# Performance work log

Hardware: AMD Instinct MI355X
Metric: run time of the kernel (lower is better)

## Reference

```python
import jax, jax.numpy as jnp
import numpy as np

B, T, H = 32, 2048, 1024

def setup_inputs() -> dict:
    key = jax.random.key(0)
    ks = jax.random.split(key, 8)
    s = 1.0 / np.sqrt(H)
    return {
        "query": jax.random.normal(ks[0], (B, H), dtype=jnp.float32),
        "values": jax.random.normal(ks[1], (B, T, H), dtype=jnp.float32),
        "Wq": jax.random.uniform(ks[2], (H, H), jnp.float32, -s, s),
        "bq": jax.random.uniform(ks[3], (H,), jnp.float32, -s, s),
        "Wv": jax.random.uniform(ks[4], (H, H), jnp.float32, -s, s),
        "bv": jax.random.uniform(ks[5], (H,), jnp.float32, -s, s),
        "Vw": jax.random.uniform(ks[6], (1, H), jnp.float32, -s, s),
        "Vb": jax.random.uniform(ks[7], (1,), jnp.float32, -s, s),
    }

def reference(query, values, Wq, bq, Wv, bv, Vw, Vb):
    # q_proj: [B,1,H], v_proj: [B,T,H]
    q_proj = (query @ Wq.T + bq)[:, None, :]
    v_proj = jnp.einsum('bth,oh->bto', values, Wv) + bv
    # score: [B,T,1] = tanh(...) @ Vw.T + Vb
    score = jnp.einsum('bth,oh->bto', jnp.tanh(q_proj + v_proj), Vw) + Vb
    attention_weights = jax.nn.softmax(score, axis=1)  # over time
    context_vector = jnp.sum(attention_weights * values, axis=1)  # [B,H]
    return (context_vector, attention_weights)
```

## Files before the change

### kernel.cpp

```cpp
#include <hip/hip_runtime.h>

#define BATCH 32
#define TT    2048
#define HH    1024
#define MTOT  (BATCH * TT)

typedef unsigned short ushort_t;
typedef short sh8 __attribute__((ext_vector_type(8)));
typedef float f4 __attribute__((ext_vector_type(4)));
typedef unsigned short us8 __attribute__((ext_vector_type(8)));

__device__ __forceinline__ ushort_t f2bf(float f) {
    unsigned u = __float_as_uint(f);
    u = (u + 0x7fffu + ((u >> 16) & 1u)) >> 16;
    return (ushort_t)u;
}
__device__ __forceinline__ float bf2f(ushort_t h) {
    return __uint_as_float(((unsigned)h) << 16);
}
__device__ __forceinline__ float fast_tanh(float x) {
    float e = __expf(2.0f * x);
    return 1.0f - 2.0f * __builtin_amdgcn_rcpf(e + 1.0f);
}

__device__ __forceinline__ void glds16(const void* g, void* l) {
    __builtin_amdgcn_global_load_lds(
        (const __attribute__((address_space(1))) void*)g,
        (__attribute__((address_space(3))) void*)l, 16, 0, 0);
}

__global__ void cvt_bf16_k(const float* __restrict__ in, ushort_t* __restrict__ out, long n) {
    long i = ((long)blockIdx.x * blockDim.x + threadIdx.x) * 8;
    if (i + 8 > n) return;
    float4 a = *(const float4*)(in + i);
    float4 b = *(const float4*)(in + i + 4);
    us8 o;
    o[0]=f2bf(a.x); o[1]=f2bf(a.y); o[2]=f2bf(a.z); o[3]=f2bf(a.w);
    o[4]=f2bf(b.x); o[5]=f2bf(b.y); o[6]=f2bf(b.z); o[7]=f2bf(b.w);
    *(us8*)(out + i) = o;
}

__global__ void qproj_k(const float* __restrict__ query, const float* __restrict__ Wq,
                        const float* __restrict__ bq, const float* __restrict__ bv,
                        float* __restrict__ qp) {
    int o = blockIdx.x, tid = threadIdx.x;
    float4 w4 = *(const float4*)(Wq + (long)o * HH + tid * 4);
    __shared__ float sm[BATCH][4];
    int wid = tid >> 6, lane = tid & 63;
    for (int b = 0; b < BATCH; ++b) {
        float4 q4 = *(const float4*)(query + (long)b * HH + tid * 4);
        float p = q4.x*w4.x + q4.y*w4.y + q4.z*w4.z + q4.w*w4.w;
        #pragma unroll
        for (int m = 1; m < 64; m <<= 1) p += __shfl_xor(p, m);
        if (lane == 0) sm[b][wid] = p;
    }
    __syncthreads();
    if (tid < BATCH) {
        float s = sm[tid][0] + sm[tid][1] + sm[tid][2] + sm[tid][3] + bq[o] + bv[o];
        qp[(long)tid * HH + o] = s;
    }
}

#define BM 128
#define BN 128
#define BK 64

__global__ __launch_bounds__(256, 2) void score_gemm_k(
    const ushort_t* __restrict__ A, const ushort_t* __restrict__ Bw,
    const float* __restrict__ qp, const float* __restrict__ Vw,
    float* __restrict__ score)
{
    __shared__ ushort_t As[BM * BK];
    __shared__ ushort_t Bs[BN * BK];
    int tid = threadIdx.x;

    int bx = blockIdx.x;
    int x  = bx & 7;
    int s  = bx >> 3;
    int nt = s & 7;
    int mt = ((s >> 3) << 3) | x;
    const long m0 = (long)mt * BM;
    const int  n0 = nt * BN;

    int wid  = tid >> 6, lane = tid & 63;
    int quad = lane >> 4, l16 = lane & 15;
    int wrow = (wid >> 1) * 64, wcol = (wid & 1) * 64;

    f4 acc[4][4] = {};

    int srow = tid >> 3;
    int sseg = tid & 7;
    int xseg = sseg ^ (srow & 7);
    const ushort_t* Ag = A  + (m0 + srow) * (long)HH + xseg * 8;
    const ushort_t* Bg = Bw + (long)(n0 + srow) * HH + xseg * 8;
    char* AsB = (char*)As;
    char* BsB = (char*)Bs;
    const int ldsOff = wid * 1024;

    for (int kt = 0; kt < HH / BK; ++kt) {
        const int kb = kt * BK;
        #pragma unroll
        for (int c = 0; c < 4; ++c) {
            glds16(Ag + (long)c * 32 * HH + kb, AsB + c * 4096 + ldsOff);
            glds16(Bg + (long)c * 32 * HH + kb, BsB + c * 4096 + ldsOff);
        }
        __syncthreads();

        sh8 af[4][2], bf[4][2];
        #pragma unroll
        for (int i = 0; i < 4; ++i) {
            int r = wrow + i * 16 + l16;
            #pragma unroll
            for (int kq = 0; kq < 2; ++kq) {
                int sg = (kq * 4 + quad) ^ (r & 7);
                af[i][kq] = *(const sh8*)(AsB + r * 128 + sg * 16);
            }
        }
        #pragma unroll
        for (int j = 0; j < 4; ++j) {
            int r = wcol + j * 16 + l16;
            #pragma unroll
            for (int kq = 0; kq < 2; ++kq) {
                int sg = (kq * 4 + quad) ^ (r & 7);
                bf[j][kq] = *(const sh8*)(BsB + r * 128 + sg * 16);
            }
        }
        #pragma unroll
        for (int kq = 0; kq < 2; ++kq)
            #pragma unroll
            for (int i = 0; i < 4; ++i)
                #pragma unroll
                for (int j = 0; j < 4; ++j)
                    acc[i][j] = __builtin_amdgcn_mfma_f32_16x16x32_bf16(
                        af[i][kq], bf[j][kq], acc[i][j], 0, 0, 0);
        __syncthreads();
    }

    int bidx = (int)(m0 >> 11);
    const float* qpb = qp + (long)bidx * HH;
    float qv[4], vw[4];
    #pragma unroll
    for (int j = 0; j < 4; ++j) {
        int cg = n0 + wcol + j * 16 + l16;
        qv[j] = qpb[cg];
        vw[j] = Vw[cg];
    }
    #pragma unroll
    for (int i = 0; i < 4; ++i) {
        #pragma unroll
        for (int r = 0; r < 4; ++r) {
            float sum = 0.0f;
            #pragma unroll
            for (int j = 0; j < 4; ++j) {
                float xv = acc[i][j][r] + qv[j];
                sum += fast_tanh(xv) * vw[j];
            }
            sum += __shfl_xor(sum, 1);
            sum += __shfl_xor(sum, 2);
            sum += __shfl_xor(sum, 4);
            sum += __shfl_xor(sum, 8);
            if (l16 == 0) {
                atomicAdd(score + m0 + wrow + i * 16 + quad * 4 + r, sum);
            }
        }
    }
}

__global__ void softmax_k(const float* __restrict__ sc, float* __restrict__ w) {
    int b = blockIdx.x, tid = threadIdx.x;
    const float* s = sc + (long)b * TT;
    float v[8];
    float4 a0 = *(const float4*)(s + tid * 8);
    float4 a1 = *(const float4*)(s + tid * 8 + 4);
    v[0]=a0.x; v[1]=a0.y; v[2]=a0.z; v[3]=a0.w;
    v[4]=a1.x; v[5]=a1.y; v[6]=a1.z; v[7]=a1.w;
    float mx = v[0];
    #pragma unroll
    for (int i = 1; i < 8; ++i) mx = fmaxf(mx, v[i]);
    #pragma unroll
    for (int m = 1; m < 64; m <<= 1) mx = fmaxf(mx, __shfl_xor(mx, m));
    __shared__ float smx[4], ssum[4];
    int wid = tid >> 6;
    if ((tid & 63) == 0) smx[wid] = mx;
    __syncthreads();
    mx = fmaxf(fmaxf(smx[0], smx[1]), fmaxf(smx[2], smx[3]));
    float sum = 0.0f;
    #pragma unroll
    for (int i = 0; i < 8; ++i) { v[i] = __expf(v[i] - mx); sum += v[i]; }
    #pragma unroll
    for (int m = 1; m < 64; m <<= 1) sum += __shfl_xor(sum, m);
    if ((tid & 63) == 0) ssum[wid] = sum;
    __syncthreads();
    sum = ssum[0] + ssum[1] + ssum[2] + ssum[3];
    float inv = 1.0f / sum;
    float4 o0 = make_float4(v[0]*inv, v[1]*inv, v[2]*inv, v[3]*inv);
    float4 o1 = make_float4(v[4]*inv, v[5]*inv, v[6]*inv, v[7]*inv);
    *(float4*)(w + (long)b * TT + tid * 8)     = o0;
    *(float4*)(w + (long)b * TT + tid * 8 + 4) = o1;
}

__global__ void context_k2(const ushort_t* __restrict__ vb, const float* __restrict__ w,
                           float* __restrict__ partial) {
    int b = blockIdx.x, tc = blockIdx.y;
    int tid = threadIdx.x;
    int toff = tid >> 7;
    int hi   = tid & 127;
    int h    = hi * 8;
    __shared__ float sw[128];
    __shared__ float red[128][8];
    if (tid < 128) sw[tid] = w[(long)b * TT + tc * 128 + tid];
    __syncthreads();

    const ushort_t* base = vb + ((long)b * TT + tc * 128 + toff) * HH + h;
    float acc[8] = {0.f,0.f,0.f,0.f,0.f,0.f,0.f,0.f};
    #pragma unroll 8
    for (int it = 0; it < 64; ++it) {
        us8 v = *(const us8*)(base + (long)it * 2 * HH);
        float wt = sw[it * 2 + toff];
        #pragma unroll
        for (int e = 0; e < 8; ++e) acc[e] += wt * bf2f(v[e]);
    }
    if (toff == 1) {
        #pragma unroll
        for (int e = 0; e < 8; ++e) red[hi][e] = acc[e];
    }
    __syncthreads();
    if (toff == 0) {
        #pragma unroll
        for (int e = 0; e < 8; ++e) acc[e] += red[hi][e];
        float* p = partial + ((long)tc * 32 + b) * HH + h;
        *(float4*)(p)     = make_float4(acc[0], acc[1], acc[2], acc[3]);
        *(float4*)(p + 4) = make_float4(acc[4], acc[5], acc[6], acc[7]);
    }
}

__global__ void context_red_k(const float* __restrict__ partial, float* __restrict__ ctx) {
    int i = blockIdx.x * 256 + threadIdx.x;
    float s = 0.f;
    #pragma unroll
    for (int tc = 0; tc < 16; ++tc) s += partial[(long)tc * 32768 + i];
    ctx[i] = s;
}

extern "C" void kernel_launch(void* const* d_in, const int* in_sizes, int n_in,
                              void* d_out, int out_size, void* d_ws, size_t ws_size,
                              hipStream_t stream) {
    const float* query  = (const float*)d_in[0];
    const float* values = (const float*)d_in[1];
    const float* Wq     = (const float*)d_in[2];
    const float* bq     = (const float*)d_in[3];
    const float* Wv     = (const float*)d_in[4];
    const float* bv     = (const float*)d_in[5];
    const float* Vw     = (const float*)d_in[6];

    char* ws = (char*)d_ws;
    ushort_t* vb   = (ushort_t*)ws;
    ushort_t* wvb  = (ushort_t*)(ws + 134217728);
    float*    qp   = (float*)   (ws + 134217728 + 2097152);
    float*    scre = (float*)   (ws + 134217728 + 2097152 + 131072);
    float*    partial = (float*)wvb;

    float* ctx  = (float*)d_out;
    float* wout = (float*)d_out + BATCH * HH;

    hipMemsetAsync(scre, 0, (size_t)MTOT * 4, stream);

    cvt_bf16_k<<<(BATCH * TT * HH) / 2048, 256, 0, stream>>>(values, vb, (long)BATCH * TT * HH);
    cvt_bf16_k<<<(HH * HH) / 2048, 256, 0, stream>>>(Wv, wvb, (long)HH * HH);

    qproj_k<<<HH, 256, 0, stream>>>(query, Wq, bq, bv, qp);

    score_gemm_k<<<(MTOT / BM) * (HH / BN), 256, 0, stream>>>(vb, wvb, qp, Vw, scre);

    softmax_k<<<BATCH, 256, 0, stream>>>(scre, wout);

    context_k2<<<dim3(BATCH, 16), 256, 0, stream>>>(vb, wout, partial);
    context_red_k<<<(BATCH * HH) / 256, 256, 0, stream>>>(partial, ctx);
}
```

Measured before the change: 569.8 us.

## Rewrite score GEMM as 256x256 double-buffered pipelined kernel with 8 waves

Replaces the 128x128 single-buffered bf16 MFMA GEMM with a 256x256 tile using 512 threads, double-buffered LDS, and a hand-scheduled ping-pong pipeline. Global-to-LDS loads for the next K slice are interleaved with MFMA quadrants, coordinated by explicit barriers, waitcnt and setprio. The goal is to hide load latency and raise data reuse per block. It uses 128KB of LDS per block, which limits occupancy and makes the code fragile about waitcnt correctness.

```diff
diff --git a/kernel.cpp b/kernel.cpp
--- a/kernel.cpp
+++ b/kernel.cpp
@@ -61,79 +61,126 @@
     }
 }
 
-#define BM 128
-#define BN 128
-#define BK 64
-
-__global__ __launch_bounds__(256, 2) void score_gemm_k(
+
+#define PBAR()  __builtin_amdgcn_s_barrier()
+#define LGKM0() asm volatile("s_waitcnt lgkmcnt(0)" ::: "memory")
+#define VMW(n)  asm volatile("s_waitcnt vmcnt(" #n ")" ::: "memory")
+#define PRIO(p) __builtin_amdgcn_s_setprio(p)
+
+__device__ __forceinline__ void stage_half(const ushort_t* __restrict__ gbase,
+                                           long row0, int kb,
+                                           char* ldsbase, int h, int w8, int lane) {
+    #pragma unroll
+    for (int c = 0; c < 2; ++c) {
+        int r  = h * 128 + c * 64 + w8 + (lane >> 3);
+        int sg = (lane & 7) ^ (r & 7);
+        glds16(gbase + (row0 + r) * (long)HH + kb + sg * 8,
+               ldsbase + (h * 128 + c * 64 + w8) * 128);
+    }
+}
+
+#define READ_A(Lp, ibase)                                                        \
+    { _Pragma("unroll") for (int i2_ = 0; i2_ < 4; ++i2_) {                      \
+        int r_ = wr * 128 + ((ibase) + i2_) * 16 + l16;                          \
+        _Pragma("unroll") for (int kq_ = 0; kq_ < 2; ++kq_)                      \
+            af[i2_][kq_] = *(const sh8*)((Lp) + r_ * 128 +                       \
+                                          ((((kq_ * 4) + quad) ^ (r_ & 7)) * 16)); } }
+
+#define READ_B(Lp, jbase)                                                        \
+    { _Pragma("unroll") for (int j2_ = 0; j2_ < 2; ++j2_) {                      \
+        int r_ = wc * 64 + ((jbase) + j2_) * 16 + l16;                           \
+        _Pragma("unroll") for (int kq_ = 0; kq_ < 2; ++kq_)                      \
+            bf[(jbase) + j2_][kq_] = *(const sh8*)((Lp) + r_ * 128 +             \
+                                          ((((kq_ * 4) + quad) ^ (r_ & 7)) * 16)); } }
+
+#define MFMA_Q(ibase, jbase)                                                     \
+    { _Pragma("unroll") for (int kq_ = 0; kq_ < 2; ++kq_) {                      \
+      _Pragma("unroll") for (int i2_ = 0; i2_ < 4; ++i2_) {                      \
+      _Pragma("unroll") for (int j2_ = 0; j2_ < 2; ++j2_) {                      \
+            acc[(ibase) + i2_][(jbase) + j2_] =                                  \
+                __builtin_amdgcn_mfma_f32_16x16x32_bf16(                         \
+                    af[i2_][kq_], bf[(jbase) + j2_][kq_],                        \
+                    acc[(ibase) + i2_][(jbase) + j2_], 0, 0, 0); } } } }
+
+__global__ __launch_bounds__(512, 2) void score_gemm_k(
     const ushort_t* __restrict__ A, const ushort_t* __restrict__ Bw,
     const float* __restrict__ qp, const float* __restrict__ Vw,
     float* __restrict__ score)
 {
-    __shared__ ushort_t As[BM * BK];
-    __shared__ ushort_t Bs[BN * BK];
-    int tid = threadIdx.x;
-
-    int bx = blockIdx.x;
-    int x  = bx & 7;
-    int s  = bx >> 3;
-    int nt = s & 7;
-    int mt = ((s >> 3) << 3) | x;
-    const long m0 = (long)mt * BM;
-    const int  n0 = nt * BN;
-
-    int wid  = tid >> 6, lane = tid & 63;
-    int quad = lane >> 4, l16 = lane & 15;
-    int wrow = (wid >> 1) * 64, wcol = (wid & 1) * 64;
-
-    f4 acc[4][4] = {};
-
-    int srow = tid >> 3;
-    int sseg = tid & 7;
-    int xseg = sseg ^ (srow & 7);
-    const ushort_t* Ag = A  + (m0 + srow) * (long)HH + xseg * 8;
-    const ushort_t* Bg = Bw + (long)(n0 + srow) * HH + xseg * 8;
-    char* AsB = (char*)As;
-    char* BsB = (char*)Bs;
-    const int ldsOff = wid * 1024;
-
-    for (int kt = 0; kt < HH / BK; ++kt) {
-        const int kb = kt * BK;
-        #pragma unroll
-        for (int c = 0; c < 4; ++c) {
-            glds16(Ag + (long)c * 32 * HH + kb, AsB + c * 4096 + ldsOff);
-            glds16(Bg + (long)c * 32 * HH + kb, BsB + c * 4096 + ldsOff);
-        }
-        __syncthreads();
-
-        sh8 af[4][2], bf[4][2];
-        #pragma unroll
-        for (int i = 0; i < 4; ++i) {
-            int r = wrow + i * 16 + l16;
-            #pragma unroll
-            for (int kq = 0; kq < 2; ++kq) {
-                int sg = (kq * 4 + quad) ^ (r & 7);
-                af[i][kq] = *(const sh8*)(AsB + r * 128 + sg * 16);
-            }
-        }
-        #pragma unroll
-        for (int j = 0; j < 4; ++j) {
-            int r = wcol + j * 16 + l16;
-            #pragma unroll
-            for (int kq = 0; kq < 2; ++kq) {
-                int sg = (kq * 4 + quad) ^ (r & 7);
-                bf[j][kq] = *(const sh8*)(BsB + r * 128 + sg * 16);
-            }
-        }
-        #pragma unroll
-        for (int kq = 0; kq < 2; ++kq)
-            #pragma unroll
-            for (int i = 0; i < 4; ++i)
-                #pragma unroll
-                for (int j = 0; j < 4; ++j)
-                    acc[i][j] = __builtin_amdgcn_mfma_f32_16x16x32_bf16(
-                        af[i][kq], bf[j][kq], acc[i][j], 0, 0, 0);
-        __syncthreads();
+    __shared__ ushort_t As[2][256 * 64];
+    __shared__ ushort_t Bs[2][256 * 64];
+    const int tid  = threadIdx.x;
+    const int w    = tid >> 6, lane = tid & 63;
+    const int quad = lane >> 4, l16 = lane & 15;
+    const int wr   = w >> 2, wc = w & 3;
+    const int w8   = w << 3;
+
+    int bx   = blockIdx.x;
+    int wgid = (bx & 7) * 128 + (bx >> 3);
+    int mt   = wgid >> 2, nt = wgid & 3;
+    const long m0 = (long)mt * 256;
+    const long n0 = (long)nt * 256;
+
+    char* As0 = (char*)&As[0][0];
+    char* As1 = (char*)&As[1][0];
+    char* Bs0 = (char*)&Bs[0][0];
+    char* Bs1 = (char*)&Bs[1][0];
+
+    f4  acc[8][4] = {};
+    sh8 af[4][2], bf[4][2];
+
+    stage_half(A,  m0, 0,  As0, 0, w8, lane);
+    stage_half(A,  m0, 0,  As0, 1, w8, lane);
+    stage_half(Bw, n0, 0,  Bs0, 0, w8, lane);
+    stage_half(Bw, n0, 0,  Bs0, 1, w8, lane);
+    stage_half(Bw, n0, 64, Bs1, 0, w8, lane);
+    stage_half(Bw, n0, 64, Bs1, 1, w8, lane);
+    VMW(4); PBAR();
+
+    for (int it = 0; it < 7; ++it) {
+        const int kb1 = (2 * it + 1) * 64;
+        const int kb2 = (2 * it + 2) * 64;
+        const int kb3 = (2 * it + 3) * 64;
+        READ_A(As0, 0); READ_B(Bs0, 0);
+        stage_half(A, m0, kb1, As1, 0, w8, lane);
+        PBAR(); LGKM0(); PRIO(1); MFMA_Q(0, 0); PRIO(0); PBAR();
+        READ_B(Bs0, 2);
+        stage_half(A, m0, kb1, As1, 1, w8, lane);
+        PBAR(); LGKM0(); PRIO(1); MFMA_Q(0, 2); PRIO(0); PBAR();
+        READ_A(As0, 4);
+        stage_half(Bw, n0, kb2, Bs0, 0, w8, lane);
+        PBAR(); LGKM0(); PRIO(1); MFMA_Q(4, 2); PRIO(0); PBAR();
+        stage_half(Bw, n0, kb2, Bs0, 1, w8, lane);
+        VMW(4); PBAR(); PRIO(1); MFMA_Q(4, 0); PRIO(0); PBAR();
+        READ_A(As1, 0); READ_B(Bs1, 0);
+        stage_half(A, m0, kb2, As0, 0, w8, lane);
+        PBAR(); LGKM0(); PRIO(1); MFMA_Q(0, 0); PRIO(0); PBAR();
+        READ_B(Bs1, 2);
+        stage_half(A, m0, kb2, As0, 1, w8, lane);
+        PBAR(); LGKM0(); PRIO(1); MFMA_Q(0, 2); PRIO(0); PBAR();
+        READ_A(As1, 4);
+        stage_half(Bw, n0, kb3, Bs1, 0, w8, lane);
+        PBAR(); LGKM0(); PRIO(1); MFMA_Q(4, 2); PRIO(0); PBAR();
+        stage_half(Bw, n0, kb3, Bs1, 1, w8, lane);
+        VMW(4); PBAR(); PRIO(1); MFMA_Q(4, 0); PRIO(0); PBAR();
+    }
+    {
+        const int kb1 = 15 * 64;
+        READ_A(As0, 0); READ_B(Bs0, 0);
+        stage_half(A, m0, kb1, As1, 0, w8, lane);
+        PBAR(); LGKM0(); PRIO(1); MFMA_Q(0, 0); PRIO(0); PBAR();
+        READ_B(Bs0, 2);
+        stage_half(A, m0, kb1, As1, 1, w8, lane);
+        PBAR(); LGKM0(); PRIO(1); MFMA_Q(0, 2); PRIO(0); PBAR();
+        READ_A(As0, 4);
+        PBAR(); LGKM0(); PRIO(1); MFMA_Q(4, 2); PRIO(0); PBAR();
+        VMW(0); PBAR(); PRIO(1); MFMA_Q(4, 0); PRIO(0); PBAR();
+        READ_A(As1, 0); READ_B(Bs1, 0);
+        PBAR(); LGKM0(); PRIO(1); MFMA_Q(0, 0); PRIO(0); PBAR();
+        READ_B(Bs1, 2);
+        PBAR(); LGKM0(); PRIO(1); MFMA_Q(0, 2); PRIO(0); PBAR();
+        READ_A(As1, 4);
+        PBAR(); LGKM0(); PRIO(1); MFMA_Q(4, 2); MFMA_Q(4, 0); PRIO(0);
     }
 
     int bidx = (int)(m0 >> 11);
@@ -141,12 +188,12 @@
     float qv[4], vw[4];
     #pragma unroll
     for (int j = 0; j < 4; ++j) {
-        int cg = n0 + wcol + j * 16 + l16;
+        int cg = (int)n0 + wc * 64 + j * 16 + l16;
         qv[j] = qpb[cg];
         vw[j] = Vw[cg];
     }
     #pragma unroll
-    for (int i = 0; i < 4; ++i) {
+    for (int i = 0; i < 8; ++i) {
         #pragma unroll
         for (int r = 0; r < 4; ++r) {
             float sum = 0.0f;
@@ -160,7 +207,7 @@
             sum += __shfl_xor(sum, 4);
             sum += __shfl_xor(sum, 8);
             if (l16 == 0) {
-                atomicAdd(score + m0 + wrow + i * 16 + quad * 4 + r, sum);
+                atomicAdd(score + m0 + wr * 128 + i * 16 + quad * 4 + r, sum);
             }
         }
     }
@@ -270,7 +317,7 @@
 
     qproj_k<<<HH, 256, 0, stream>>>(query, Wq, bq, bv, qp);
 
-    score_gemm_k<<<(MTOT / BM) * (HH / BN), 256, 0, stream>>>(vb, wvb, qp, Vw, scre);
+    score_gemm_k<<<(MTOT / 256) * (HH / 256), 512, 0, stream>>>(vb, wvb, qp, Vw, scre);
 
     softmax_k<<<BATCH, 256, 0, stream>>>(scre, wout);
 
```

Result: slower. 597.1 us (+4.8%).
